# Performance work log

Hardware: AMD Instinct MI355X
Metric: run time of the kernel (lower is better)

The kernel has to match this reference:

```python
import jax, jax.numpy as jnp
import numpy as np

N = 50000      # nodes per side
E = 1000000    # edges
D = 256        # input_dim
H, C = 2, 32   # heads, out_channels


def setup_inputs() -> dict:
    key = jax.random.key(0)
    ks = jax.random.split(key, 8)
    h_x = jax.random.normal(ks[0], (N, D), dtype=jnp.float32)
    t_x = jax.random.normal(ks[1], (N, D), dtype=jnp.float32)
    src = jax.random.randint(ks[2], (E,), 0, N)
    dst = jax.random.randint(ks[3], (E,), 0, N)
    # PyG GATConv removes self-pairs before re-adding self loops; keep shapes
    # static by ensuring no accidental src==dst pairs.
    dst = jnp.where(dst == src, (dst + 1) % N, dst)
    edge_index = jnp.stack([src, dst]).astype(jnp.int64)
    glorot = float(np.sqrt(6.0 / (D + H * C)))
    W_src = jax.random.uniform(ks[4], (D, H * C), jnp.float32, -glorot, glorot)
    W_dst = jax.random.uniform(ks[5], (D, H * C), jnp.float32, -glorot, glorot)
    ga = float(np.sqrt(6.0 / (1 + C)))
    att_src = jax.random.uniform(ks[6], (H, C), jnp.float32, -ga, ga)
    att_dst = jax.random.uniform(ks[7], (H, C), jnp.float32, -ga, ga)
    bias = jnp.zeros((H * C,), jnp.float32)
    return {"h_x": h_x, "t_x": t_x, "edge_index": edge_index,
            "W_src": W_src, "W_dst": W_dst,
            "att_src": att_src, "att_dst": att_dst, "bias": bias}


def _gat(x_src, x_dst, src, dst, W_src, W_dst, att_src, att_dst, bias):
    Ns, Nd = x_src.shape[0], x_dst.shape[0]
    # self loops on min(Ns, Nd) nodes (PyG bipartite default)
    loops = jnp.arange(min(Ns, Nd))
    src = jnp.concatenate([src, loops])
    dst = jnp.concatenate([dst, loops])
    xs = (x_src @ W_src).reshape(Ns, H, C)   # [Ns,H,C]
    xd = (x_dst @ W_dst).reshape(Nd, H, C)   # [Nd,H,C]
    a_s = (xs * att_src).sum(-1)             # [Ns,H]
    a_d = (xd * att_dst).sum(-1)             # [Nd,H]
    alpha = jax.nn.leaky_relu(a_s[src] + a_d[dst], 0.2)  # [E+N,H]
    amax = jax.ops.segment_max(alpha, dst, num_segments=Nd)
    alpha = jnp.exp(alpha - amax[dst])
    denom = jax.ops.segment_sum(alpha, dst, num_segments=Nd)
    alpha = alpha / (denom[dst] + 1e-16)
    msg = xs[src] * alpha[:, :, None]        # [E+N,H,C]
    out = jax.ops.segment_sum(msg, dst, num_segments=Nd)
    return out.reshape(Nd, H * C) + bias


def reference(h_x, t_x, edge_index, W_src, W_dst, att_src, att_dst, bias):
    h_in = jax.nn.elu(h_x)
    t_in = jax.nn.elu(t_x)
    t_rep = _gat(h_in, t_in, edge_index[0], edge_index[1],
                 W_src, W_dst, att_src, att_dst, bias)
    h_rep = _gat(t_in, h_in, edge_index[1], edge_index[0],
                 W_src, W_dst, att_src, att_dst, bias)
    return (h_rep, t_rep)
```

## Files before the change

kernel.cpp:

```cpp
#include <hip/hip_runtime.h>
#include <hip/hip_bf16.h>
#include <cstdint>

#define DD 256
#define HC 64
#define LRELU 0.2f
#define SH 6
#define NBMAX 1024
#define CAP 3072

__device__ __forceinline__ float lrelu(float x) { return fmaxf(x, LRELU * x); }
__device__ __forceinline__ float eluf(float x) { return x > 0.f ? x : (expf(x) - 1.f); }

__global__ void prep_kernel(const void* ei, const float* __restrict__ Wsrc,
                            const float* __restrict__ Wdst,
                            const float* __restrict__ att_src,
                            const float* __restrict__ att_dst,
                            float* __restrict__ weff, int* __restrict__ flag) {
    int t = threadIdx.x;
    if (t == 0) {
        const unsigned* u = (const unsigned*)ei;
        int all0 = 1;
        for (int j = 1; j < 64; j += 2) all0 &= (u[j] == 0u);
        *flag = all0;
    }
    if (t < DD) {
        float s0 = 0.f, s1 = 0.f, d0 = 0.f, d1 = 0.f;
        for (int c = 0; c < 32; ++c) {
            s0 += Wsrc[t * HC + c]      * att_src[c];
            s1 += Wsrc[t * HC + 32 + c] * att_src[32 + c];
            d0 += Wdst[t * HC + c]      * att_dst[c];
            d1 += Wdst[t * HC + 32 + c] * att_dst[32 + c];
        }
        weff[t * 4 + 0] = s0; weff[t * 4 + 1] = s1;
        weff[t * 4 + 2] = d0; weff[t * 4 + 3] = d1;
    }
}

__global__ __launch_bounds__(256) void hist_kernel(const void* ei, int E, int NB,
                                                   const int* __restrict__ flag,
                                                   int* __restrict__ bcnt) {
    __shared__ int lc[2 * NBMAX];
    for (int t = threadIdx.x; t < 2 * NB; t += 256) lc[t] = 0;
    __syncthreads();
    const bool f64 = (*flag != 0);
    int stride = gridDim.x * 256;
    for (int i = blockIdx.x * 256 + threadIdx.x; i < E; i += stride) {
        int s, d;
        if (f64) { const long long* p = (const long long*)ei; s = (int)p[i]; d = (int)p[E + i]; }
        else     { const int* p = (const int*)ei;             s = p[i];      d = p[E + i]; }
        atomicAdd(&lc[d >> SH], 1);
        atomicAdd(&lc[NB + (s >> SH)], 1);
    }
    __syncthreads();
    for (int t = threadIdx.x; t < 2 * NB; t += 256)
        if (lc[t]) atomicAdd(&bcnt[t], lc[t]);
}

__global__ __launch_bounds__(256) void bscan_kernel(const int* __restrict__ bcnt, int NB,
                                                    int* __restrict__ boff,
                                                    int* __restrict__ cursor) {
    int g = blockIdx.x;
    const int* c = bcnt + g * NB;
    int* off = boff + g * (NB + 1);
    int* cur = cursor + g * NB;
    __shared__ int psum[256];
    int t = threadIdx.x;
    int cpt = (NB + 255) / 256;
    int b0 = t * cpt;
    int s = 0;
    for (int j = 0; j < cpt; ++j) { int b = b0 + j; if (b < NB) s += c[b]; }
    psum[t] = s;
    __syncthreads();
    for (int d2 = 1; d2 < 256; d2 <<= 1) {
        int v = (t >= d2) ? psum[t - d2] : 0;
        __syncthreads();
        psum[t] += v;
        __syncthreads();
    }
    int run = psum[t] - s;
    for (int j = 0; j < cpt; ++j) {
        int b = b0 + j;
        if (b < NB) { off[b] = run; cur[b] = run; run += c[b]; }
    }
    if (t == 255) off[NB] = psum[255];
}

__global__ __launch_bounds__(256) void bscatter_kernel(const void* ei, int E, int NB,
                                                       const int* __restrict__ flag,
                                                       int* __restrict__ cursor,
                                                       unsigned* __restrict__ bins0,
                                                       unsigned* __restrict__ bins1) {
    __shared__ int lc[2 * NBMAX];
    for (int t = threadIdx.x; t < 2 * NB; t += 256) lc[t] = 0;
    __syncthreads();
    const bool f64 = (*flag != 0);
    int stride = gridDim.x * 256;
    for (int i = blockIdx.x * 256 + threadIdx.x; i < E; i += stride) {
        int s, d;
        if (f64) { const long long* p = (const long long*)ei; s = (int)p[i]; d = (int)p[E + i]; }
        else     { const int* p = (const int*)ei;             s = p[i];      d = p[E + i]; }
        atomicAdd(&lc[d >> SH], 1);
        atomicAdd(&lc[NB + (s >> SH)], 1);
    }
    __syncthreads();
    for (int t = threadIdx.x; t < 2 * NB; t += 256) {
        int cvt = lc[t];
        lc[t] = cvt ? atomicAdd(&cursor[t], cvt) : 0;
    }
    __syncthreads();
    for (int i = blockIdx.x * 256 + threadIdx.x; i < E; i += stride) {
        int s, d;
        if (f64) { const long long* p = (const long long*)ei; s = (int)p[i]; d = (int)p[E + i]; }
        else     { const int* p = (const int*)ei;             s = p[i];      d = p[E + i]; }
        int p0 = atomicAdd(&lc[d >> SH], 1);
        bins0[p0] = ((unsigned)(d & 63) << 16) | (unsigned)s;
        int p1 = atomicAdd(&lc[NB + (s >> SH)], 1);
        bins1[p1] = ((unsigned)(s & 63) << 16) | (unsigned)d;
    }
}

__global__ __launch_bounds__(256) void gemm_proj_kernel(
    const float* __restrict__ Xh, const float* __restrict__ Xt,
    const float* __restrict__ Wsrc, const float* __restrict__ weff,
    float* __restrict__ xs_h, float* __restrict__ xs_t,
    float* __restrict__ as_h, float* __restrict__ ad_h,
    float* __restrict__ as_t, float* __restrict__ ad_t, int nrows) {

    const float* X = blockIdx.y ? Xt : Xh;
    float* xs  = blockIdx.y ? xs_t : xs_h;
    float* as_ = blockIdx.y ? as_t : as_h;
    float* ad_ = blockIdx.y ? ad_t : ad_h;

    __shared__ float Xc[128][36];
    __shared__ float Wc[32][72];
    __shared__ float Wec[4][40];

    const int tid  = threadIdx.x;
    const int row0 = blockIdx.x * 128;

    const int g  = tid >> 4;
    const int c0 = (tid & 15) * 4;
    const int er = tid >> 1;
    const int ec = (tid & 1) * 2;

    float acc[8][4];
#pragma unroll
    for (int i = 0; i < 8; ++i)
#pragma unroll
        for (int j = 0; j < 4; ++j) acc[i][j] = 0.f;
    float ea0 = 0.f, ea1 = 0.f;

    for (int kc = 0; kc < 8; ++kc) {
        {
            int r = tid >> 3, cq = tid & 7;
#pragma unroll
            for (int rr = 0; rr < 4; ++rr) {
                int row = row0 + r + rr * 32;
                float4 v = make_float4(0.f, 0.f, 0.f, 0.f);
                if (row < nrows) {
                    v = *(const float4*)(X + (size_t)row * DD + kc * 32 + cq * 4);
                    v.x = eluf(v.x); v.y = eluf(v.y); v.z = eluf(v.z); v.w = eluf(v.w);
                }
                *(float4*)&Xc[r + rr * 32][cq * 4] = v;
            }
        }
        {
#pragma unroll
            for (int q = 0; q < 2; ++q) {
                int idx = tid + q * 256;
                int k = idx >> 4, cf = idx & 15;
                *(float4*)&Wc[k][cf * 4] =
                    *(const float4*)(Wsrc + (size_t)(kc * 32 + k) * HC + cf * 4);
            }
            if (tid < 128) {
                int k = tid >> 2, j = tid & 3;
                Wec[j][k] = weff[(kc * 32 + k) * 4 + j];
            }
        }
        __syncthreads();

#pragma unroll
        for (int kq = 0; kq < 8; ++kq) {
            float4 w0 = *(const float4*)&Wc[kq * 4 + 0][c0];
            float4 w1 = *(const float4*)&Wc[kq * 4 + 1][c0];
            float4 w2 = *(const float4*)&Wc[kq * 4 + 2][c0];
            float4 w3 = *(const float4*)&Wc[kq * 4 + 3][c0];
#pragma unroll
            for (int i = 0; i < 8; ++i) {
                float4 xv = *(const float4*)&Xc[g + i * 16][kq * 4];
                acc[i][0] = fmaf(xv.x, w0.x, acc[i][0]);
                acc[i][1] = fmaf(xv.x, w0.y, acc[i][1]);
                acc[i][2] = fmaf(xv.x, w0.z, acc[i][2]);
                acc[i][3] = fmaf(xv.x, w0.w, acc[i][3]);
                acc[i][0] = fmaf(xv.y, w1.x, acc[i][0]);
                acc[i][1] = fmaf(xv.y, w1.y, acc[i][1]);
                acc[i][2] = fmaf(xv.y, w1.z, acc[i][2]);
                acc[i][3] = fmaf(xv.y, w1.w, acc[i][3]);
                acc[i][0] = fmaf(xv.z, w2.x, acc[i][0]);
                acc[i][1] = fmaf(xv.z, w2.y, acc[i][1]);
                acc[i][2] = fmaf(xv.z, w2.z, acc[i][2]);
                acc[i][3] = fmaf(xv.z, w2.w, acc[i][3]);
                acc[i][0] = fmaf(xv.w, w3.x, acc[i][0]);
                acc[i][1] = fmaf(xv.w, w3.y, acc[i][1]);
                acc[i][2] = fmaf(xv.w, w3.z, acc[i][2]);
                acc[i][3] = fmaf(xv.w, w3.w, acc[i][3]);
            }
        }
#pragma unroll
        for (int kq = 0; kq < 8; ++kq) {
            float4 xv = *(const float4*)&Xc[er][kq * 4];
            float4 u0 = *(const float4*)&Wec[ec][kq * 4];
            float4 u1 = *(const float4*)&Wec[ec + 1][kq * 4];
            ea0 = fmaf(xv.x, u0.x, ea0); ea0 = fmaf(xv.y, u0.y, ea0);
            ea0 = fmaf(xv.z, u0.z, ea0); ea0 = fmaf(xv.w, u0.w, ea0);
            ea1 = fmaf(xv.x, u1.x, ea1); ea1 = fmaf(xv.y, u1.y, ea1);
            ea1 = fmaf(xv.z, u1.z, ea1); ea1 = fmaf(xv.w, u1.w, ea1);
        }
        __syncthreads();
    }

#pragma unroll
    for (int i = 0; i < 8; ++i) {
        int row = row0 + g + i * 16;
        if (row < nrows)
            *(float4*)(xs + (size_t)row * HC + c0) =
                make_float4(acc[i][0], acc[i][1], acc[i][2], acc[i][3]);
    }
    {
        int row = row0 + er;
        if (row < nrows) {
            if (ec == 0) { as_[row * 2 + 0] = ea0; as_[row * 2 + 1] = ea1; }
            else         { ad_[row * 2 + 0] = ea0; ad_[row * 2 + 1] = ea1; }
        }
    }
}

__global__ __launch_bounds__(256) void gat_kernel(
    const unsigned* __restrict__ bins0, const unsigned* __restrict__ bins1,
    const int* __restrict__ boff, int NB,
    const float* __restrict__ xs_h, const float* __restrict__ xs_t,
    const float* __restrict__ as_h, const float* __restrict__ ad_h,
    const float* __restrict__ as_t, const float* __restrict__ ad_t,
    const float* __restrict__ bias, float* __restrict__ out, int N) {

    int g = blockIdx.y;
    int b = blockIdx.x;
    const unsigned* bins = g ? bins1 : bins0;
    const int* off = boff + g * (NB + 1);
    const float *xs, *as_, *ad_;
    float* o;
    if (g == 0) { xs = xs_h; as_ = as_h; ad_ = ad_t; o = out + (size_t)N * HC; }
    else        { xs = xs_t; as_ = as_t; ad_ = ad_h; o = out; }

    __shared__ int cnt64[64];
    __shared__ int lofs[65];
    __shared__ int lpos[64];
    __shared__ unsigned srt[CAP];

    int base = off[b];
    int cnt  = off[b + 1] - base;
    int tid  = threadIdx.x;
    bool fits = (cnt <= CAP);

    if (fits) {
        if (tid < 64) cnt64[tid] = 0;
        __syncthreads();
        for (int i = tid; i < cnt; i += 256)
            atomicAdd(&cnt64[bins[base + i] >> 16], 1);
        __syncthreads();
        if (tid == 0) {
            int r = 0;
            for (int k = 0; k < 64; ++k) { lofs[k] = r; r += cnt64[k]; }
            lofs[64] = r;
        }
        __syncthreads();
        if (tid < 64) lpos[tid] = lofs[tid];
        __syncthreads();
        for (int i = tid; i < cnt; i += 256) {
            unsigned v = bins[base + i];
            int p = atomicAdd(&lpos[v >> 16], 1);
            srt[p] = v & 0xffffu;
        }
        __syncthreads();
    }

    int wave = tid >> 6, lane = tid & 63, h = lane >> 5;
    const float* xsl = xs + lane;
    int node0 = b << SH;

    for (int q = 0; q < 16; ++q) {
        int nl = wave * 16 + q;
        int n  = node0 + nl;
        if (n >= N) break;
        float adn = ad_[n * 2 + h];
        float dn = 0.f, acc = 0.f;
        {
            float ex = __expf(lrelu(as_[n * 2 + h] + adn));
            dn += ex;
            acc += ex * xsl[(size_t)n * HC];
        }
        if (fits) {
            int e = lofs[nl], end = lofs[nl + 1];
            int npre = min(end - e, (4 - (e & 3)) & 3);
            for (int i = 0; i < npre; ++i, ++e) {
                int s = (int)srt[e];
                float ex = __expf(lrelu(as_[s * 2 + h] + adn));
                dn += ex;
                acc = fmaf(ex, xsl[(size_t)s * HC], acc);
            }
            for (; e + 4 <= end; e += 4) {
                uint4 s4 = *(const uint4*)&srt[e];
                float A0 = as_[s4.x * 2 + h], A1 = as_[s4.y * 2 + h];
                float A2 = as_[s4.z * 2 + h], A3 = as_[s4.w * 2 + h];
                float X0 = xsl[(size_t)s4.x * HC], X1 = xsl[(size_t)s4.y * HC];
                float X2 = xsl[(size_t)s4.z * HC], X3 = xsl[(size_t)s4.w * HC];
                float e0 = __expf(lrelu(A0 + adn));
                float e1 = __expf(lrelu(A1 + adn));
                float e2 = __expf(lrelu(A2 + adn));
                float e3 = __expf(lrelu(A3 + adn));
                dn += e0; acc = fmaf(e0, X0, acc);
                dn += e1; acc = fmaf(e1, X1, acc);
                dn += e2; acc = fmaf(e2, X2, acc);
                dn += e3; acc = fmaf(e3, X3, acc);
            }
            for (; e < end; ++e) {
                int s = (int)srt[e];
                float ex = __expf(lrelu(as_[s * 2 + h] + adn));
                dn += ex;
                acc = fmaf(ex, xsl[(size_t)s * HC], acc);
            }
        } else {
            for (int e = 0; e < cnt; ++e) {
                unsigned v = bins[base + e];
                if ((int)(v >> 16) == nl) {
                    int s = (int)(v & 0xffffu);
                    float ex = __expf(lrelu(as_[s * 2 + h] + adn));
                    dn += ex;
                    acc = fmaf(ex, xsl[(size_t)s * HC], acc);
                }
            }
        }
        o[(size_t)n * HC + lane] = acc / (dn + 1e-16f) + bias[lane];
    }
}

extern "C" void kernel_launch(void* const* d_in, const int* in_sizes, int n_in,
                              void* d_out, int out_size, void* d_ws, size_t ws_size,
                              hipStream_t stream) {
    const float* h_x     = (const float*)d_in[0];
    const float* t_x     = (const float*)d_in[1];
    const void*  ei      = d_in[2];
    const float* Wsrc    = (const float*)d_in[3];
    const float* Wdst    = (const float*)d_in[4];
    const float* att_src = (const float*)d_in[5];
    const float* att_dst = (const float*)d_in[6];
    const float* bias    = (const float*)d_in[7];

    const int N = in_sizes[0] / DD;
    const int E = in_sizes[2] / 2;
    const int NB = (N + 63) >> SH;
    float* out = (float*)d_out;

    char* w = (char*)d_ws;
    auto alloc = [&](size_t bytes) -> char* {
        char* p = w;
        w += (bytes + 255) & ~(size_t)255;
        return p;
    };
    int*      bcnt   = (int*)alloc((size_t)2 * NB * 4);
    int*      boff   = (int*)alloc((size_t)2 * (NB + 1) * 4);
    int*      cursor = (int*)alloc((size_t)2 * NB * 4);
    unsigned* bins0  = (unsigned*)alloc((size_t)E * 4);
    unsigned* bins1  = (unsigned*)alloc((size_t)E * 4);
    float*    xs_h   = (float*)alloc((size_t)N * HC * 4);
    float*    xs_t   = (float*)alloc((size_t)N * HC * 4);
    float*    as_h   = (float*)alloc((size_t)N * 2 * 4);
    float*    ad_h   = (float*)alloc((size_t)N * 2 * 4);
    float*    as_t   = (float*)alloc((size_t)N * 2 * 4);
    float*    ad_t   = (float*)alloc((size_t)N * 2 * 4);
    float*    weff   = (float*)alloc((size_t)DD * 4 * 4);
    int*      flag   = (int*)alloc(256);

    hipMemsetAsync(bcnt, 0, (size_t)2 * NB * 4, stream);

    prep_kernel<<<1, 256, 0, stream>>>(ei, Wsrc, Wdst, att_src, att_dst, weff, flag);

    hist_kernel<<<256, 256, 0, stream>>>(ei, E, NB, flag, bcnt);

    bscan_kernel<<<2, 256, 0, stream>>>(bcnt, NB, boff, cursor);

    bscatter_kernel<<<128, 256, 0, stream>>>(ei, E, NB, flag, cursor, bins0, bins1);

    dim3 gg((N + 127) / 128, 2);
    gemm_proj_kernel<<<gg, 256, 0, stream>>>(h_x, t_x, Wsrc, weff,
                                             xs_h, xs_t, as_h, ad_h, as_t, ad_t, N);

    dim3 ga(NB, 2);
    gat_kernel<<<ga, 256, 0, stream>>>(bins0, bins1, boff, NB,
                                       xs_h, xs_t, as_h, ad_h, as_t, ad_t,
                                       bias, out, N);
}
```

Baseline: 355.6 us.

## Reuse per-block histograms in scatter and retile projection GEMM with fused attention columns

Result: slower. 374.0 us (+5.2%).

```diff
diff --git a/kernel.cpp b/kernel.cpp
--- a/kernel.cpp
+++ b/kernel.cpp
@@ -8,6 +8,7 @@
 #define SH 6
 #define NBMAX 1024
 #define CAP 3072
+#define PB 256
 
 __device__ __forceinline__ float lrelu(float x) { return fmaxf(x, LRELU * x); }
 __device__ __forceinline__ float eluf(float x) { return x > 0.f ? x : (expf(x) - 1.f); }
@@ -39,12 +40,13 @@
 
 __global__ __launch_bounds__(256) void hist_kernel(const void* ei, int E, int NB,
                                                    const int* __restrict__ flag,
-                                                   int* __restrict__ bcnt) {
+                                                   int* __restrict__ bcnt,
+                                                   int* __restrict__ blkcnt) {
     __shared__ int lc[2 * NBMAX];
     for (int t = threadIdx.x; t < 2 * NB; t += 256) lc[t] = 0;
     __syncthreads();
     const bool f64 = (*flag != 0);
-    int stride = gridDim.x * 256;
+    int stride = PB * 256;
     for (int i = blockIdx.x * 256 + threadIdx.x; i < E; i += stride) {
         int s, d;
         if (f64) { const long long* p = (const long long*)ei; s = (int)p[i]; d = (int)p[E + i]; }
@@ -53,8 +55,12 @@
         atomicAdd(&lc[NB + (s >> SH)], 1);
     }
     __syncthreads();
-    for (int t = threadIdx.x; t < 2 * NB; t += 256)
-        if (lc[t]) atomicAdd(&bcnt[t], lc[t]);
+    int* myblk = blkcnt + (size_t)blockIdx.x * 2 * NB;
+    for (int t = threadIdx.x; t < 2 * NB; t += 256) {
+        int c = lc[t];
+        myblk[t] = c;
+        if (c) atomicAdd(&bcnt[t], c);
+    }
 }
 
 __global__ __launch_bounds__(256) void bscan_kernel(const int* __restrict__ bcnt, int NB,
@@ -89,26 +95,18 @@
 __global__ __launch_bounds__(256) void bscatter_kernel(const void* ei, int E, int NB,
                                                        const int* __restrict__ flag,
                                                        int* __restrict__ cursor,
+                                                       const int* __restrict__ blkcnt,
                                                        unsigned* __restrict__ bins0,
                                                        unsigned* __restrict__ bins1) {
     __shared__ int lc[2 * NBMAX];
-    for (int t = threadIdx.x; t < 2 * NB; t += 256) lc[t] = 0;
+    const int* myblk = blkcnt + (size_t)blockIdx.x * 2 * NB;
+    for (int t = threadIdx.x; t < 2 * NB; t += 256) {
+        int c = myblk[t];
+        lc[t] = c ? atomicAdd(&cursor[t], c) : 0;
+    }
     __syncthreads();
     const bool f64 = (*flag != 0);
-    int stride = gridDim.x * 256;
-    for (int i = blockIdx.x * 256 + threadIdx.x; i < E; i += stride) {
-        int s, d;
-        if (f64) { const long long* p = (const long long*)ei; s = (int)p[i]; d = (int)p[E + i]; }
-        else     { const int* p = (const int*)ei;             s = p[i];      d = p[E + i]; }
-        atomicAdd(&lc[d >> SH], 1);
-        atomicAdd(&lc[NB + (s >> SH)], 1);
-    }
-    __syncthreads();
-    for (int t = threadIdx.x; t < 2 * NB; t += 256) {
-        int cvt = lc[t];
-        lc[t] = cvt ? atomicAdd(&cursor[t], cvt) : 0;
-    }
-    __syncthreads();
+    int stride = PB * 256;
     for (int i = blockIdx.x * 256 + threadIdx.x; i < E; i += stride) {
         int s, d;
         if (f64) { const long long* p = (const long long*)ei; s = (int)p[i]; d = (int)p[E + i]; }
@@ -120,7 +118,7 @@
     }
 }
 
-__global__ __launch_bounds__(256) void gemm_proj_kernel(
+__global__ __launch_bounds__(256, 5) void gemm_proj_kernel(
     const float* __restrict__ Xh, const float* __restrict__ Xt,
     const float* __restrict__ Wsrc, const float* __restrict__ weff,
     float* __restrict__ xs_h, float* __restrict__ xs_t,
@@ -132,106 +130,84 @@
     float* as_ = blockIdx.y ? as_t : as_h;
     float* ad_ = blockIdx.y ? ad_t : ad_h;
 
-    __shared__ float Xc[128][36];
-    __shared__ float Wc[32][72];
-    __shared__ float Wec[4][40];
+    __shared__ float Xc[64][33];
+    __shared__ float Wc[68][36];
 
     const int tid  = threadIdx.x;
-    const int row0 = blockIdx.x * 128;
-
-    const int g  = tid >> 4;
-    const int c0 = (tid & 15) * 4;
-    const int er = tid >> 1;
-    const int ec = (tid & 1) * 2;
-
-    float acc[8][4];
-#pragma unroll
-    for (int i = 0; i < 8; ++i)
-#pragma unroll
-        for (int j = 0; j < 4; ++j) acc[i][j] = 0.f;
-    float ea0 = 0.f, ea1 = 0.f;
+    const int row0 = blockIdx.x * 64;
+    const int team = tid >> 6;
+    const int r    = tid & 63;
+    const int col0 = team * 17;
+
+    const int sr = tid >> 2;
+    const int sq = tid & 3;
+
+    float acc[17];
+#pragma unroll
+    for (int j = 0; j < 17; ++j) acc[j] = 0.f;
 
     for (int kc = 0; kc < 8; ++kc) {
         {
-            int r = tid >> 3, cq = tid & 7;
-#pragma unroll
-            for (int rr = 0; rr < 4; ++rr) {
-                int row = row0 + r + rr * 32;
-                float4 v = make_float4(0.f, 0.f, 0.f, 0.f);
-                if (row < nrows) {
-                    v = *(const float4*)(X + (size_t)row * DD + kc * 32 + cq * 4);
-                    v.x = eluf(v.x); v.y = eluf(v.y); v.z = eluf(v.z); v.w = eluf(v.w);
-                }
-                *(float4*)&Xc[r + rr * 32][cq * 4] = v;
-            }
-        }
-        {
-#pragma unroll
-            for (int q = 0; q < 2; ++q) {
-                int idx = tid + q * 256;
-                int k = idx >> 4, cf = idx & 15;
-                *(float4*)&Wc[k][cf * 4] =
-                    *(const float4*)(Wsrc + (size_t)(kc * 32 + k) * HC + cf * 4);
-            }
-            if (tid < 128) {
-                int k = tid >> 2, j = tid & 3;
-                Wec[j][k] = weff[(kc * 32 + k) * 4 + j];
-            }
+            int row = row0 + sr;
+            float4 a = make_float4(0.f, 0.f, 0.f, 0.f), b = a;
+            if (row < nrows) {
+                const float* p = X + (size_t)row * DD + kc * 32 + sq * 8;
+                a = *(const float4*)p;
+                b = *(const float4*)(p + 4);
+                a.x = eluf(a.x); a.y = eluf(a.y); a.z = eluf(a.z); a.w = eluf(a.w);
+                b.x = eluf(b.x); b.y = eluf(b.y); b.z = eluf(b.z); b.w = eluf(b.w);
+            }
+            float* q = &Xc[sr][sq * 8];
+            q[0] = a.x; q[1] = a.y; q[2] = a.z; q[3] = a.w;
+            q[4] = b.x; q[5] = b.y; q[6] = b.z; q[7] = b.w;
+        }
+#pragma unroll
+        for (int q = 0; q < 2; ++q) {
+            int idx = tid + q * 256;
+            int k = idx >> 4, cq = idx & 15;
+            float4 wv = *(const float4*)(Wsrc + (size_t)(kc * 32 + k) * HC + cq * 4);
+            Wc[cq * 4 + 0][k] = wv.x;
+            Wc[cq * 4 + 1][k] = wv.y;
+            Wc[cq * 4 + 2][k] = wv.z;
+            Wc[cq * 4 + 3][k] = wv.w;
+        }
+        if (tid < 32) {
+            float4 wv = *(const float4*)(weff + (size_t)(kc * 32 + tid) * 4);
+            Wc[64][tid] = wv.x; Wc[65][tid] = wv.y;
+            Wc[66][tid] = wv.z; Wc[67][tid] = wv.w;
         }
         __syncthreads();
 
 #pragma unroll
         for (int kq = 0; kq < 8; ++kq) {
-            float4 w0 = *(const float4*)&Wc[kq * 4 + 0][c0];
-            float4 w1 = *(const float4*)&Wc[kq * 4 + 1][c0];
-            float4 w2 = *(const float4*)&Wc[kq * 4 + 2][c0];
-            float4 w3 = *(const float4*)&Wc[kq * 4 + 3][c0];
-#pragma unroll
-            for (int i = 0; i < 8; ++i) {
-                float4 xv = *(const float4*)&Xc[g + i * 16][kq * 4];
-                acc[i][0] = fmaf(xv.x, w0.x, acc[i][0]);
-                acc[i][1] = fmaf(xv.x, w0.y, acc[i][1]);
-                acc[i][2] = fmaf(xv.x, w0.z, acc[i][2]);
-                acc[i][3] = fmaf(xv.x, w0.w, acc[i][3]);
-                acc[i][0] = fmaf(xv.y, w1.x, acc[i][0]);
-                acc[i][1] = fmaf(xv.y, w1.y, acc[i][1]);
-                acc[i][2] = fmaf(xv.y, w1.z, acc[i][2]);
-                acc[i][3] = fmaf(xv.y, w1.w, acc[i][3]);
-                acc[i][0] = fmaf(xv.z, w2.x, acc[i][0]);
-                acc[i][1] = fmaf(xv.z, w2.y, acc[i][1]);
-                acc[i][2] = fmaf(xv.z, w2.z, acc[i][2]);
-                acc[i][3] = fmaf(xv.z, w2.w, acc[i][3]);
-                acc[i][0] = fmaf(xv.w, w3.x, acc[i][0]);
-                acc[i][1] = fmaf(xv.w, w3.y, acc[i][1]);
-                acc[i][2] = fmaf(xv.w, w3.z, acc[i][2]);
-                acc[i][3] = fmaf(xv.w, w3.w, acc[i][3]);
-            }
-        }
-#pragma unroll
-        for (int kq = 0; kq < 8; ++kq) {
-            float4 xv = *(const float4*)&Xc[er][kq * 4];
-            float4 u0 = *(const float4*)&Wec[ec][kq * 4];
-            float4 u1 = *(const float4*)&Wec[ec + 1][kq * 4];
-            ea0 = fmaf(xv.x, u0.x, ea0); ea0 = fmaf(xv.y, u0.y, ea0);
-            ea0 = fmaf(xv.z, u0.z, ea0); ea0 = fmaf(xv.w, u0.w, ea0);
-            ea1 = fmaf(xv.x, u1.x, ea1); ea1 = fmaf(xv.y, u1.y, ea1);
-            ea1 = fmaf(xv.z, u1.z, ea1); ea1 = fmaf(xv.w, u1.w, ea1);
-        }
-        __syncthreads();
-    }
-
-#pragma unroll
-    for (int i = 0; i < 8; ++i) {
-        int row = row0 + g + i * 16;
-        if (row < nrows)
-            *(float4*)(xs + (size_t)row * HC + c0) =
-                make_float4(acc[i][0], acc[i][1], acc[i][2], acc[i][3]);
-    }
-    {
-        int row = row0 + er;
-        if (row < nrows) {
-            if (ec == 0) { as_[row * 2 + 0] = ea0; as_[row * 2 + 1] = ea1; }
-            else         { ad_[row * 2 + 0] = ea0; ad_[row * 2 + 1] = ea1; }
+            float x0 = Xc[r][kq * 4 + 0];
+            float x1 = Xc[r][kq * 4 + 1];
+            float x2 = Xc[r][kq * 4 + 2];
+            float x3 = Xc[r][kq * 4 + 3];
+#pragma unroll
+            for (int j = 0; j < 17; ++j) {
+                float4 wv = *(const float4*)&Wc[col0 + j][kq * 4];
+                acc[j] = fmaf(x0, wv.x, acc[j]);
+                acc[j] = fmaf(x1, wv.y, acc[j]);
+                acc[j] = fmaf(x2, wv.z, acc[j]);
+                acc[j] = fmaf(x3, wv.w, acc[j]);
+            }
+        }
+        __syncthreads();
+    }
+
+    int row = row0 + r;
+    if (row < nrows) {
+        if (team < 3) {
+#pragma unroll
+            for (int j = 0; j < 17; ++j)
+                xs[(size_t)row * HC + col0 + j] = acc[j];
+        } else {
+#pragma unroll
+            for (int j = 0; j < 13; ++j)
+                xs[(size_t)row * HC + 51 + j] = acc[j];
+            as_[row * 2 + 0] = acc[13]; as_[row * 2 + 1] = acc[14];
+            ad_[row * 2 + 0] = acc[15]; ad_[row * 2 + 1] = acc[16];
         }
     }
 }
@@ -371,6 +347,7 @@
     int*      bcnt   = (int*)alloc((size_t)2 * NB * 4);
     int*      boff   = (int*)alloc((size_t)2 * (NB + 1) * 4);
     int*      cursor = (int*)alloc((size_t)2 * NB * 4);
+    int*      blkcnt = (int*)alloc((size_t)PB * 2 * NB * 4);
     unsigned* bins0  = (unsigned*)alloc((size_t)E * 4);
     unsigned* bins1  = (unsigned*)alloc((size_t)E * 4);
     float*    xs_h   = (float*)alloc((size_t)N * HC * 4);
@@ -386,13 +363,14 @@
 
     prep_kernel<<<1, 256, 0, stream>>>(ei, Wsrc, Wdst, att_src, att_dst, weff, flag);
 
-    hist_kernel<<<256, 256, 0, stream>>>(ei, E, NB, flag, bcnt);
+    hist_kernel<<<PB, 256, 0, stream>>>(ei, E, NB, flag, bcnt, blkcnt);
 
     bscan_kernel<<<2, 256, 0, stream>>>(bcnt, NB, boff, cursor);
 
-    bscatter_kernel<<<128, 256, 0, stream>>>(ei, E, NB, flag, cursor, bins0, bins1);
-
-    dim3 gg((N + 127) / 128, 2);
+    bscatter_kernel<<<PB, 256, 0, stream>>>(ei, E, NB, flag, cursor, blkcnt,
+                                            bins0, bins1);
+
+    dim3 gg((N + 63) / 64, 2);
     gemm_proj_kernel<<<gg, 256, 0, stream>>>(h_x, t_x, Wsrc, weff,
                                              xs_h, xs_t, as_h, ad_h, as_t, ad_t, N);
 
```
